# Performance work log

Hardware: AMD Instinct MI355X
Metric: run time of the kernel (lower is better)

The kernel has to match this reference:

```python
import jax, jax.numpy as jnp
import numpy as np


def setup_inputs() -> dict:
    key = jax.random.key(0)
    k1, k2, k3 = jax.random.split(key, 3)
    B, E, L, D = 32, 256, 2048, 256
    doc_state = jax.random.normal(k1, (B, L, D), dtype=jnp.float32)
    entity_mapping = jax.random.uniform(k2, (B, E, L), dtype=jnp.float32)
    entity_lens = jax.random.uniform(k3, (B, E), dtype=jnp.float32)
    return {"doc_state": doc_state, "entity_mapping": entity_mapping, "entity_lens": entity_lens}


def reference(doc_state, entity_mapping, entity_lens):
    # Original: (entity_mapping[:, :, :, None] * doc_state[:, None, :, :]).sum(2) / entity_lens[:, :, None]
    # This is a batched contraction over L; express as einsum to avoid the
    # huge [B, E, L, D] intermediate.
    summed = jnp.einsum('bel,bld->bed', entity_mapping, doc_state)  # [B, E, D]
    return summed / entity_lens[:, :, None]
```

## Files before the change

kernel.cpp:

```cpp
#include <hip/hip_runtime.h>
#include <stdint.h>

#define B_ 32
#define E_ 256
#define L_ 2048
#define D_ 256

#define BE 128
#define BD 256
#define BK 32
#define KS 4
#define KCHUNK (L_ / KS)
#define NKT (KCHUNK / BK)

#define SLAB_FLOATS ((size_t)B_ * E_ * D_)
#define WS_NEED     (KS * SLAB_FLOATS * 4)

typedef __attribute__((ext_vector_type(4))) float  f32x4;
typedef __attribute__((ext_vector_type(8))) short  s16x8;

__device__ __forceinline__ void cvt_hilo1(float x, short &h, short &l) {
    unsigned u = __builtin_bit_cast(unsigned, x);
    h = (short)(u >> 16);
    float hf = __builtin_bit_cast(float, u & 0xFFFF0000u);
    unsigned r = __builtin_bit_cast(unsigned, x - hf);
    l = (short)(r >> 16);
}

__global__ void zero_out_kernel(f32x4* __restrict__ out) {
    out[(size_t)blockIdx.x * 256 + threadIdx.x] = f32x4{0.f, 0.f, 0.f, 0.f};
}

__global__ __launch_bounds__(256)
void reduce_kernel(const f32x4* __restrict__ ws, const float* __restrict__ lens,
                   f32x4* __restrict__ out) {
    const size_t i = (size_t)blockIdx.x * 256 + threadIdx.x;
    const float lv = lens[i >> 6];
    f32x4 s0 = ws[i];
    f32x4 s1 = ws[i +     (SLAB_FLOATS / 4)];
    f32x4 s2 = ws[i + 2 * (SLAB_FLOATS / 4)];
    f32x4 s3 = ws[i + 3 * (SLAB_FLOATS / 4)];
    f32x4 r;
    #pragma unroll
    for (int c = 0; c < 4; ++c) r[c] = (s0[c] + s1[c] + s2[c] + s3[c]) / lv;
    out[i] = r;
}

__device__ __forceinline__ void gload16(const float* g, float* l) {
    __builtin_amdgcn_global_load_lds(
        (const __attribute__((address_space(1))) void*)g,
        (__attribute__((address_space(3))) void*)l, 16, 0, 0);
}

#define ISSUE_TILE(AB, BB, K0)                                                 \
    {                                                                          \
        _Pragma("unroll")                                                      \
        for (int i = 0; i < 2; ++i) {                                          \
            const int r_ = w * 16 + i * 8 + (lane >> 3);                       \
            const int q_ = (lane & 7) ^ (r_ & 7);                              \
            gload16(Ag + (size_t)r_ * L_ + (K0) + q_ * 4, (AB) + (w * 2 + i) * 256); \
        }                                                                      \
        _Pragma("unroll")                                                      \
        for (int i = 0; i < 4; ++i) {                                          \
            const int k_ = w * 4 + i;                                          \
            const int ds_ = 4 * (lane ^ (((k_ >> 3) & 3) << 2));               \
            gload16(Sg + (size_t)((K0) + k_) * D_ + ds_, (BB) + k_ * 256);     \
        }                                                                      \
    }

#define COMPUTE(AB, BB)                                                        \
    {                                                                          \
        f32x4 afl[4], afh[4];                                                  \
        _Pragma("unroll")                                                      \
        for (int mi = 0; mi < 4; ++mi) {                                       \
            const int row_ = eo + mi * 16 + ml;                                \
            afl[mi] = *(const f32x4*)((AB) + row_ * 32 + a_o1);                \
            afh[mi] = *(const f32x4*)((AB) + row_ * 32 + a_o2);                \
        }                                                                      \
        float bfv[4][8];                                                       \
        _Pragma("unroll")                                                      \
        for (int ni = 0; ni < 4; ++ni)                                         \
            _Pragma("unroll")                                                  \
            for (int j = 0; j < 8; ++j)                                        \
                bfv[ni][j] = (BB)[b_o[ni] + j * 256];                          \
        s16x8 bh[4], bl[4];                                                    \
        _Pragma("unroll")                                                      \
        for (int ni = 0; ni < 4; ++ni)                                         \
            _Pragma("unroll")                                                  \
            for (int j = 0; j < 8; ++j) {                                      \
                short hh, ll; cvt_hilo1(bfv[ni][j], hh, ll);                   \
                bh[ni][j] = hh; bl[ni][j] = ll;                                \
            }                                                                  \
        __builtin_amdgcn_s_setprio(1);                                         \
        _Pragma("unroll")                                                      \
        for (int mi = 0; mi < 4; ++mi) {                                       \
            s16x8 ah, al;                                                      \
            _Pragma("unroll")                                                  \
            for (int q = 0; q < 4; ++q) { short hh, ll; cvt_hilo1(afl[mi][q], hh, ll); ah[q] = hh; al[q] = ll; } \
            _Pragma("unroll")                                                  \
            for (int q = 0; q < 4; ++q) { short hh, ll; cvt_hilo1(afh[mi][q], hh, ll); ah[4 + q] = hh; al[4 + q] = ll; } \
            _Pragma("unroll")                                                  \
            for (int ni = 0; ni < 4; ++ni) {                                   \
                acc[mi][ni] = __builtin_amdgcn_mfma_f32_16x16x32_bf16(ah, bh[ni], acc[mi][ni], 0, 0, 0); \
                acc[mi][ni] = __builtin_amdgcn_mfma_f32_16x16x32_bf16(ah, bl[ni], acc[mi][ni], 0, 0, 0); \
                acc[mi][ni] = __builtin_amdgcn_mfma_f32_16x16x32_bf16(al, bh[ni], acc[mi][ni], 0, 0, 0); \
            }                                                                  \
        }                                                                      \
        __builtin_amdgcn_s_setprio(0);                                         \
    }

#define STEP_FULL(ABC, BBC, ABN, BBN)                                          \
    {                                                                          \
        ISSUE_TILE(ABN, BBN, knext)                                            \
        knext += BK;                                                           \
        COMPUTE(ABC, BBC)                                                      \
        asm volatile("s_waitcnt vmcnt(6)" ::: "memory");                       \
        __builtin_amdgcn_s_barrier();                                          \
        asm volatile("" ::: "memory");                                         \
    }

template <int WS>
__global__ __launch_bounds__(512, 2)
void mean_pool_kernel(const float* __restrict__ doc,
                      const float* __restrict__ emap,
                      const float* __restrict__ lens,
                      float* __restrict__ out,
                      float* __restrict__ wsp) {
    __shared__ __align__(16) float Asm[3][BE * BK];
    __shared__ __align__(16) float Bsm[3][BK * BD];

    const int t  = threadIdx.x;
    const int bi = blockIdx.x;
    const int r_  = bi & 7;
    const int q_  = bi >> 3;
    const int ks  = r_ & 3;
    const int b   = (q_ >> 1) * 2 + (r_ >> 2);
    const int e0  = (q_ & 1) * BE;

    const float* Ag = emap + ((size_t)b * E_ + e0) * L_ + ks * KCHUNK;
    const float* Sg = doc  + (size_t)b * L_ * D_ + (size_t)ks * KCHUNK * D_;

    const int lane = t & 63;
    const int w    = t >> 6;
    const int eo   = (w & 1) * 64;
    const int dq   = (w >> 1) * 64;
    const int ml   = lane & 15;
    const int kg   = lane >> 4;

    const int a_o1 = (((2 * kg)    ) ^ (ml & 7)) * 4;
    const int a_o2 = (((2 * kg) | 1) ^ (ml & 7)) * 4;
    int b_o[4];
    #pragma unroll
    for (int ni = 0; ni < 4; ++ni)
        b_o[ni] = kg * 2048 + dq + ((ni ^ kg) * 16) + ml;

    float* const A0 = &Asm[0][0];  float* const B0 = &Bsm[0][0];
    float* const A1 = &Asm[1][0];  float* const B1 = &Bsm[1][0];
    float* const A2 = &Asm[2][0];  float* const B2 = &Bsm[2][0];

    f32x4 acc[4][4] = {};

    ISSUE_TILE(A0, B0, 0)
    ISSUE_TILE(A1, B1, BK)
    asm volatile("s_waitcnt vmcnt(6)" ::: "memory");
    __builtin_amdgcn_s_barrier();
    asm volatile("" ::: "memory");

    int knext = 2 * BK;

    #pragma unroll 1
    for (int g = 0; g < 4; ++g) {
        STEP_FULL(A0, B0, A2, B2)
        STEP_FULL(A1, B1, A0, B0)
        STEP_FULL(A2, B2, A1, B1)
    }
    STEP_FULL(A0, B0, A2, B2)
    STEP_FULL(A1, B1, A0, B0)

    COMPUTE(A2, B2)
    asm volatile("s_waitcnt vmcnt(0)" ::: "memory");
    __builtin_amdgcn_s_barrier();
    asm volatile("" ::: "memory");

    COMPUTE(A0, B0)

    if (WS) {
        float* wsb = wsp + (size_t)ks * SLAB_FLOATS
                         + ((size_t)(b * E_ + e0)) * D_ + dq;
        #pragma unroll
        for (int mi = 0; mi < 4; ++mi) {
            #pragma unroll
            for (int rr = 0; rr < 4; ++rr) {
                const int er = eo + mi * 16 + kg * 4 + rr;
                #pragma unroll
                for (int ni = 0; ni < 4; ++ni)
                    wsb[(size_t)er * D_ + ni * 16 + ml] = acc[mi][ni][rr];
            }
        }
    } else {
        const float* lensB = lens + b * E_ + e0;
        #pragma unroll
        for (int mi = 0; mi < 4; ++mi) {
            #pragma unroll
            for (int rr = 0; rr < 4; ++rr) {
                const int er = eo + mi * 16 + kg * 4 + rr;
                const float lv = lensB[er];
                #pragma unroll
                for (int ni = 0; ni < 4; ++ni)
                    atomicAdd(&out[((size_t)(b * E_ + e0 + er)) * D_ + dq + ni * 16 + ml],
                              acc[mi][ni][rr] / lv);
            }
        }
    }
}

extern "C" void kernel_launch(void* const* d_in, const int* in_sizes, int n_in,
                              void* d_out, int out_size, void* d_ws, size_t ws_size,
                              hipStream_t stream) {
    const float* doc  = (const float*)d_in[0];
    const float* emap = (const float*)d_in[1];
    const float* lens = (const float*)d_in[2];
    float* out = (float*)d_out;
    float* ws  = (float*)d_ws;

    dim3 pgrid(B_ * (E_ / BE) * (D_ / BD) * KS);
    dim3 pblock(512);

    if (ws_size >= (size_t)WS_NEED) {
        hipLaunchKernelGGL((mean_pool_kernel<1>), pgrid, pblock, 0, stream,
                           doc, emap, lens, out, ws);
        hipLaunchKernelGGL(reduce_kernel,
                           dim3((unsigned)(SLAB_FLOATS / 4 / 256)), dim3(256), 0, stream,
                           (const f32x4*)ws, lens, (f32x4*)out);
    } else {
        zero_out_kernel<<<dim3(out_size / (4 * 256)), dim3(256), 0, stream>>>((f32x4*)out);
        hipLaunchKernelGGL((mean_pool_kernel<0>), pgrid, pblock, 0, stream,
                           doc, emap, lens, out, ws);
    }
}
```

Measured before the change: 172.7 us.

## Restructure to per-wave private A tiles with direct-to-register B loads

Replaces the 512-thread block and its shared triple-buffered A/B tiles with 256-thread blocks of 128x128 output tiles. Each wave now double-buffers its own private slice of the entity_mapping tile in LDS, and doc_state values are loaded straight from global memory into registers one step ahead. This drops block-wide barriers and the B staging in LDS. In exchange, doc_state is read redundantly by each wave (no sharing across the E dimension within a block), and the grid doubles to 1024 smaller blocks.

```diff
diff --git a/kernel.cpp b/kernel.cpp
--- a/kernel.cpp
+++ b/kernel.cpp
@@ -6,11 +6,9 @@
 #define L_ 2048
 #define D_ 256
 
-#define BE 128
-#define BD 256
-#define BK 32
 #define KS 4
 #define KCHUNK (L_ / KS)
+#define BK 32
 #define NKT (KCHUNK / BK)
 
 #define SLAB_FLOATS ((size_t)B_ * E_ * D_)
@@ -52,53 +50,50 @@
         (__attribute__((address_space(3))) void*)l, 16, 0, 0);
 }
 
-#define ISSUE_TILE(AB, BB, K0)                                                 \
+#define ISSUE_A(BUF, K0)                                                       \
     {                                                                          \
         _Pragma("unroll")                                                      \
-        for (int i = 0; i < 2; ++i) {                                          \
-            const int r_ = w * 16 + i * 8 + (lane >> 3);                       \
-            const int q_ = (lane & 7) ^ (r_ & 7);                              \
-            gload16(Ag + (size_t)r_ * L_ + (K0) + q_ * 4, (AB) + (w * 2 + i) * 256); \
+        for (int i = 0; i < 8; ++i) {                                          \
+            const int r_ = i * 8 + a_r8;                                       \
+            const int q_ = a_q ^ (r_ & 7);                                     \
+            gload16(AgW + (size_t)r_ * L_ + (K0) + q_ * 4, (BUF) + i * 256);   \
         }                                                                      \
-        _Pragma("unroll")                                                      \
-        for (int i = 0; i < 4; ++i) {                                          \
-            const int k_ = w * 4 + i;                                          \
-            const int ds_ = 4 * (lane ^ (((k_ >> 3) & 3) << 2));               \
-            gload16(Sg + (size_t)((K0) + k_) * D_ + ds_, (BB) + k_ * 256);     \
-        }                                                                      \
-    }
-
-#define COMPUTE(AB, BB)                                                        \
+    }
+
+#define LOADB(PB, K0)                                                          \
     {                                                                          \
-        f32x4 afl[4], afh[4];                                                  \
-        _Pragma("unroll")                                                      \
-        for (int mi = 0; mi < 4; ++mi) {                                       \
-            const int row_ = eo + mi * 16 + ml;                                \
-            afl[mi] = *(const f32x4*)((AB) + row_ * 32 + a_o1);                \
-            afh[mi] = *(const f32x4*)((AB) + row_ * 32 + a_o2);                \
-        }                                                                      \
-        float bfv[4][8];                                                       \
         _Pragma("unroll")                                                      \
         for (int ni = 0; ni < 4; ++ni)                                         \
             _Pragma("unroll")                                                  \
             for (int j = 0; j < 8; ++j)                                        \
-                bfv[ni][j] = (BB)[b_o[ni] + j * 256];                          \
+                PB[ni][j] = Sg[(size_t)((K0) + kg * 8 + j) * D_ + ni * 16 + ml]; \
+    }
+
+#define STEP(K, BUFC, BUFN)                                                    \
+    {                                                                          \
+        if ((K) + 1 < NKT) ISSUE_A(BUFN, ((K) + 1) * BK)                       \
+                 \
+        asm volatile("s_waitcnt vmcnt(8)" ::: "memory");                       \
         s16x8 bh[4], bl[4];                                                    \
         _Pragma("unroll")                                                      \
         for (int ni = 0; ni < 4; ++ni)                                         \
             _Pragma("unroll")                                                  \
             for (int j = 0; j < 8; ++j) {                                      \
-                short hh, ll; cvt_hilo1(bfv[ni][j], hh, ll);                   \
+                short hh, ll; cvt_hilo1(pbv[ni][j], hh, ll);                   \
                 bh[ni][j] = hh; bl[ni][j] = ll;                                \
             }                                                                  \
+        if ((K) + 1 < NKT) LOADB(pbv, ((K) + 1) * BK)                          \
         __builtin_amdgcn_s_setprio(1);                                         \
         _Pragma("unroll")                                                      \
         for (int mi = 0; mi < 4; ++mi) {                                       \
+            const int row_ = mi * 16 + ml;                                     \
+            const f32x4 alo = *(const f32x4*)((BUFC) + row_ * 32 + a_c1);      \
+            const f32x4 ahi = *(const f32x4*)((BUFC) + row_ * 32 + a_c2);      \
             s16x8 ah, al;                                                      \
             _Pragma("unroll")                                                  \
-            for (int q = 0; q < 4; ++q) { short hh, ll; cvt_hilo1(afl[mi][q], hh, ll); ah[q] = hh; al[q] = ll; } \
-            _Pragma("unroll")                                                  \
-            for (int q = 0; q < 4; ++q) { short hh, ll; cvt_hilo1(afh[mi][q], hh, ll); ah[4 + q] = hh; al[4 + q] = ll; } \
+            for (int q = 0; q < 4; ++q) { short hh, ll; cvt_hilo1(alo[q], hh, ll); ah[q] = hh; al[q] = ll; } \
+            _Pragma("unroll")                                                  \
+            for (int q = 0; q < 4; ++q) { short hh, ll; cvt_hilo1(ahi[q], hh, ll); ah[4 + q] = hh; al[4 + q] = ll; } \
             _Pragma("unroll")                                                  \
             for (int ni = 0; ni < 4; ++ni) {                                   \
                 acc[mi][ni] = __builtin_amdgcn_mfma_f32_16x16x32_bf16(ah, bh[ni], acc[mi][ni], 0, 0, 0); \
@@ -109,36 +104,21 @@
         __builtin_amdgcn_s_setprio(0);                                         \
     }
 
-#define STEP_FULL(ABC, BBC, ABN, BBN)                                          \
-    {                                                                          \
-        ISSUE_TILE(ABN, BBN, knext)                                            \
-        knext += BK;                                                           \
-        COMPUTE(ABC, BBC)                                                      \
-        asm volatile("s_waitcnt vmcnt(6)" ::: "memory");                       \
-        __builtin_amdgcn_s_barrier();                                          \
-        asm volatile("" ::: "memory");                                         \
-    }
-
 template <int WS>
-__global__ __launch_bounds__(512, 2)
+__global__ __launch_bounds__(256, 2)
 void mean_pool_kernel(const float* __restrict__ doc,
                       const float* __restrict__ emap,
                       const float* __restrict__ lens,
                       float* __restrict__ out,
                       float* __restrict__ wsp) {
-    __shared__ __align__(16) float Asm[3][BE * BK];
-    __shared__ __align__(16) float Bsm[3][BK * BD];
-
-    const int t  = threadIdx.x;
-    const int bi = blockIdx.x;
-    const int r_  = bi & 7;
-    const int q_  = bi >> 3;
-    const int ks  = r_ & 3;
-    const int b   = (q_ >> 1) * 2 + (r_ >> 2);
-    const int e0  = (q_ & 1) * BE;
-
-    const float* Ag = emap + ((size_t)b * E_ + e0) * L_ + ks * KCHUNK;
-    const float* Sg = doc  + (size_t)b * L_ * D_ + (size_t)ks * KCHUNK * D_;
+    __shared__ __align__(16) float Apl[4][2][2048];
+
+    const int t   = threadIdx.x;
+    const int blk = blockIdx.x;
+    const int ks  = blk & 3;
+    const int dB  = (blk >> 2) & 1;
+    const int eB  = (blk >> 3) & 1;
+    const int b   = blk >> 4;
 
     const int lane = t & 63;
     const int w    = t >> 6;
@@ -147,67 +127,52 @@
     const int ml   = lane & 15;
     const int kg   = lane >> 4;
 
-    const int a_o1 = (((2 * kg)    ) ^ (ml & 7)) * 4;
-    const int a_o2 = (((2 * kg) | 1) ^ (ml & 7)) * 4;
-    int b_o[4];
-    #pragma unroll
-    for (int ni = 0; ni < 4; ++ni)
-        b_o[ni] = kg * 2048 + dq + ((ni ^ kg) * 16) + ml;
-
-    float* const A0 = &Asm[0][0];  float* const B0 = &Bsm[0][0];
-    float* const A1 = &Asm[1][0];  float* const B1 = &Bsm[1][0];
-    float* const A2 = &Asm[2][0];  float* const B2 = &Bsm[2][0];
+    const float* AgW = emap + ((size_t)(b * E_ + eB * 128 + eo)) * L_ + ks * KCHUNK;
+    const float* Sg  = doc  + (size_t)b * L_ * D_ + (size_t)ks * KCHUNK * D_ + dB * 128 + dq;
+
+    const int a_r8 = lane >> 3;
+    const int a_q  = lane & 7;
+    const int a_c1 = (((2 * kg)    ) ^ (ml & 7)) * 4;
+    const int a_c2 = (((2 * kg) | 1) ^ (ml & 7)) * 4;
+
+    float* const Ab0 = &Apl[w][0][0];
+    float* const Ab1 = &Apl[w][1][0];
 
     f32x4 acc[4][4] = {};
-
-    ISSUE_TILE(A0, B0, 0)
-    ISSUE_TILE(A1, B1, BK)
-    asm volatile("s_waitcnt vmcnt(6)" ::: "memory");
-    __builtin_amdgcn_s_barrier();
-    asm volatile("" ::: "memory");
-
-    int knext = 2 * BK;
-
-    #pragma unroll 1
-    for (int g = 0; g < 4; ++g) {
-        STEP_FULL(A0, B0, A2, B2)
-        STEP_FULL(A1, B1, A0, B0)
-        STEP_FULL(A2, B2, A1, B1)
-    }
-    STEP_FULL(A0, B0, A2, B2)
-    STEP_FULL(A1, B1, A0, B0)
-
-    COMPUTE(A2, B2)
-    asm volatile("s_waitcnt vmcnt(0)" ::: "memory");
-    __builtin_amdgcn_s_barrier();
-    asm volatile("" ::: "memory");
-
-    COMPUTE(A0, B0)
+    float pbv[4][8];
+
+    ISSUE_A(Ab0, 0)
+    LOADB(pbv, 0)
+
+    for (int kt = 0; kt < NKT; kt += 2) {
+        STEP(kt,     Ab0, Ab1)
+        STEP(kt + 1, Ab1, Ab0)
+    }
 
     if (WS) {
         float* wsb = wsp + (size_t)ks * SLAB_FLOATS
-                         + ((size_t)(b * E_ + e0)) * D_ + dq;
+                         + ((size_t)(b * E_ + eB * 128 + eo)) * D_ + dB * 128 + dq;
         #pragma unroll
         for (int mi = 0; mi < 4; ++mi) {
             #pragma unroll
             for (int rr = 0; rr < 4; ++rr) {
-                const int er = eo + mi * 16 + kg * 4 + rr;
+                const int er = mi * 16 + kg * 4 + rr;
                 #pragma unroll
                 for (int ni = 0; ni < 4; ++ni)
                     wsb[(size_t)er * D_ + ni * 16 + ml] = acc[mi][ni][rr];
             }
         }
     } else {
-        const float* lensB = lens + b * E_ + e0;
         #pragma unroll
         for (int mi = 0; mi < 4; ++mi) {
             #pragma unroll
             for (int rr = 0; rr < 4; ++rr) {
-                const int er = eo + mi * 16 + kg * 4 + rr;
-                const float lv = lensB[er];
+                const int er = mi * 16 + kg * 4 + rr;
+                const float lv = lens[b * E_ + eB * 128 + eo + er];
                 #pragma unroll
                 for (int ni = 0; ni < 4; ++ni)
-                    atomicAdd(&out[((size_t)(b * E_ + e0 + er)) * D_ + dq + ni * 16 + ml],
+                    atomicAdd(&out[((size_t)(b * E_ + eB * 128 + eo + er)) * D_
+                                   + dB * 128 + dq + ni * 16 + ml],
                               acc[mi][ni][rr] / lv);
             }
         }
@@ -223,18 +188,18 @@
     float* out = (float*)d_out;
     float* ws  = (float*)d_ws;
 
-    dim3 pgrid(B_ * (E_ / BE) * (D_ / BD) * KS);
-    dim3 pblock(512);
+    dim3 grid(B_ * KS * (E_ / 128) * (D_ / 128));
+    dim3 block(256);
 
     if (ws_size >= (size_t)WS_NEED) {
-        hipLaunchKernelGGL((mean_pool_kernel<1>), pgrid, pblock, 0, stream,
+        hipLaunchKernelGGL((mean_pool_kernel<1>), grid, block, 0, stream,
                            doc, emap, lens, out, ws);
         hipLaunchKernelGGL(reduce_kernel,
                            dim3((unsigned)(SLAB_FLOATS / 4 / 256)), dim3(256), 0, stream,
                            (const f32x4*)ws, lens, (f32x4*)out);
     } else {
         zero_out_kernel<<<dim3(out_size / (4 * 256)), dim3(256), 0, stream>>>((f32x4*)out);
-        hipLaunchKernelGGL((mean_pool_kernel<0>), pgrid, pblock, 0, stream,
+        hipLaunchKernelGGL((mean_pool_kernel<0>), grid, block, 0, stream,
                            doc, emap, lens, out, ws);
     }
 }
```

After: 175.3 us. About the same (+1.5%).
